# Kernel tuning notes

Hardware: AMD Instinct MI355X
Metric: run time of the kernel (lower is better)

Reference implementation:

```python
import jax, jax.numpy as jnp
import numpy as np

B, P, L = 256, 16, 4
NUM_ENTITY, NUM_NODE = 500000, 512
E, C1, C2 = 128, 512, 256


def setup_inputs() -> dict:
    key = jax.random.key(0)
    ks = jax.random.split(key, 13)
    inp = {
        "start_ids": jax.random.randint(ks[0], (B, P), 0, NUM_ENTITY, dtype=jnp.int32),
        "end_ids": jax.random.randint(ks[1], (B, P), 0, NUM_ENTITY, dtype=jnp.int32),
        "module_ids": jax.random.randint(ks[2], (B, P, L), 0, NUM_NODE, dtype=jnp.int32),
        "counts": jax.random.randint(ks[3], (B, P), 1, 10, dtype=jnp.int32),
        # learned parameters
        "embed": jax.random.normal(ks[4], (NUM_ENTITY, E), dtype=jnp.float32) * 0.02,
        "W": jax.random.normal(ks[5], (NUM_NODE, E, E), dtype=jnp.float32) * (1.0 / np.sqrt(E)),
        "b": jax.random.normal(ks[6], (NUM_NODE, E), dtype=jnp.float32) * 0.01,
        "W1": jax.random.normal(ks[7], (C1, 2 * E), dtype=jnp.float32) * (1.0 / np.sqrt(2 * E)),
        "b1": jnp.zeros((C1,), jnp.float32),
        "W2": jax.random.normal(ks[8], (C2, C1), dtype=jnp.float32) * (1.0 / np.sqrt(C1)),
        "b2": jnp.zeros((C2,), jnp.float32),
        "W3": jax.random.normal(ks[9], (1, C2), dtype=jnp.float32) * (1.0 / np.sqrt(C2)),
        "b3": jnp.zeros((1,), jnp.float32),
    }
    return inp


def reference(start_ids, end_ids, module_ids, counts, embed, W, b, W1, b1, W2, b2, W3, b3):
    # Embed path endpoints: [B, P, E]
    x = embed[start_ids]
    y = embed[end_ids]

    # Apply the same per-node Linear chain to both endpoint embeddings.
    # Scan over the L path steps; gather the step's weight matrices per path.
    def step(carry, mids):  # mids: [B, P]
        x, y = carry
        Wg = W[mids]            # [B, P, E, E] (out, in)
        bg = b[mids]            # [B, P, E]
        x = jnp.einsum('bpi,bpoi->bpo', x, Wg) + bg
        y = jnp.einsum('bpi,bpoi->bpo', y, Wg) + bg
        return (x, y), None

    (x, y), _ = jax.lax.scan(step, (x, y), jnp.transpose(module_ids, (2, 0, 1)))

    feat = jnp.concatenate([x, y], axis=-1)          # [B, P, 2E]
    c = counts.astype(feat.dtype)                    # path multiplicities
    pooled = jnp.einsum('bp,bpf->bf', c, feat) / jnp.sum(c, axis=1, keepdims=True)

    h = jax.nn.relu(pooled @ W1.T + b1)
    h = jax.nn.relu(h @ W2.T + b2)
    out = jax.nn.sigmoid(h @ W3.T + b3)              # [B, 1]
    return out
```

## Files before the change

kernel.cpp:

```cpp
#include <hip/hip_runtime.h>
#include <math.h>

#define BB 256
#define PP 16
#define LL 4
#define EE 128
#define NPATH (BB*PP)
#define NMOD 512
#define CC1 512
#define CC2 256

#define WS_STATE   0
#define WS_CNT     (NPATH*2*EE*4)
#define WS_OFF     (WS_CNT  + LL*NMOD*4)
#define WS_CUR     (WS_OFF  + LL*NMOD*4)
#define WS_LISTS   (WS_CUR  + LL*NMOD*4)
#define WS_POOLED  (WS_LISTS + LL*NPATH*4)
#define WS_H1      (WS_POOLED + BB*2*EE*4)
#define WS_H2      (WS_H1 + BB*CC1*4)
#define WS_END     (WS_H2 + BB*CC2*4)

#define FMA4(A, S, Wv) do{ (A).x=fmaf((S),(Wv).x,(A).x); (A).y=fmaf((S),(Wv).y,(A).y); \
                           (A).z=fmaf((S),(Wv).z,(A).z); (A).w=fmaf((S),(Wv).w,(A).w);}while(0)

__global__ __launch_bounds__(256) void k_zero(int* __restrict__ cnt) {
    cnt[blockIdx.x*256 + threadIdx.x] = 0;
}

__global__ __launch_bounds__(256) void k_seed(
    const int* __restrict__ start_ids, const int* __restrict__ end_ids,
    const int* __restrict__ module_ids, const float* __restrict__ embed,
    float* __restrict__ state, int* __restrict__ cnt)
{
    const int bp = blockIdx.x, t = threadIdx.x;
    const int id = (t < EE) ? start_ids[bp] : end_ids[bp];
    state[(size_t)bp*256 + t] = embed[(size_t)id*EE + (t & (EE-1))];
    if (t < LL) atomicAdd(&cnt[t*NMOD + module_ids[bp*LL + t]], 1);
}

__global__ void k_scan(const int* __restrict__ cnt, int* __restrict__ off,
                       int* __restrict__ cur)
{
    const int l = blockIdx.x, t = threadIdx.x;
    __shared__ int s[NMOD];
    const int c = cnt[l*NMOD + t];
    s[t] = c; __syncthreads();
    for (int d = 1; d < NMOD; d <<= 1) {
        const int v = (t >= d) ? s[t-d] : 0;
        __syncthreads();
        s[t] += v;
        __syncthreads();
    }
    const int excl = s[t] - c;
    off[l*NMOD + t] = excl;
    cur[l*NMOD + t] = excl;
}

__global__ __launch_bounds__(256) void k_scatter(
    const int* __restrict__ module_ids, int* __restrict__ cur,
    int* __restrict__ lists)
{
    const int gid = blockIdx.x*256 + threadIdx.x;
    const int bp = gid >> 2, l = gid & 3;
    const int m = module_ids[gid];
    const int pos = atomicAdd(&cur[l*NMOD + m], 1);
    lists[l*NPATH + pos] = bp;
}

__global__ __launch_bounds__(256) void k_step(
    const int l, const float* __restrict__ W, const float* __restrict__ bvec,
    const int* __restrict__ cnt, const int* __restrict__ off,
    const int* __restrict__ lists, float* __restrict__ state)
{
    __shared__ float Wt[128*64];
    __shared__ float vb[32*128];
    const int m = blockIdx.x, t = threadIdx.x;
    const int n = cnt[l*NMOD + m];
    if (n == 0) return;
    const int* lst = lists + l*NPATH + off[l*NMOD + m];
    const int nr = 2*n;
    const int c = t & 15;
    const int g = t >> 4;
    const float4* state4c = (const float4*)state;

    for (int base = 0; base < nr; base += 32) {
        __syncthreads();
        #pragma unroll
        for (int it = 0; it < 4; ++it) {
            const int flat = it*256 + t;
            const int row = flat >> 5, c4 = flat & 31;
            const int pc = c4 ^ ((row >> 1) & 3);
            float4 v = make_float4(0.f, 0.f, 0.f, 0.f);
            const int r = base + row;
            if (r < nr) {
                const int pv = lst[r >> 1]*2 + (r & 1);
                v = state4c[pv*32 + c4];
            }
            ((float4*)vb)[row*32 + pc] = v;
        }
        for (int ch = 0; ch < 2; ++ch) {
            __syncthreads();
            {
                const int oc = t & 63, kh = t >> 6;
                const float4* Wr = (const float4*)(W + ((size_t)m*128 + ch*64 + oc)*128);
                #pragma unroll
                for (int it = 0; it < 8; ++it) {
                    const int k0 = kh*32 + it*4;
                    const float4 wv = Wr[k0 >> 2];
                    Wt[(k0+0)*64 + oc] = wv.x;
                    Wt[(k0+1)*64 + oc] = wv.y;
                    Wt[(k0+2)*64 + oc] = wv.z;
                    Wt[(k0+3)*64 + oc] = wv.w;
                }
            }
            __syncthreads();
            float4 acc0 = make_float4(0,0,0,0), acc1 = make_float4(0,0,0,0);
            const int row0 = g*2, row1 = g*2 + 1;
            const int sw = g & 3;
            #pragma unroll 4
            for (int k0 = 0; k0 < 128; k0 += 4) {
                const int q = k0 >> 2;
                const float4 w0 = ((const float4*)Wt)[(k0+0)*16 + c];
                const float4 w1 = ((const float4*)Wt)[(k0+1)*16 + c];
                const float4 w2 = ((const float4*)Wt)[(k0+2)*16 + c];
                const float4 w3 = ((const float4*)Wt)[(k0+3)*16 + c];
                const float4 va = ((const float4*)vb)[row0*32 + (q ^ sw)];
                const float4 vy = ((const float4*)vb)[row1*32 + (q ^ sw)];
                FMA4(acc0, va.x, w0); FMA4(acc0, va.y, w1);
                FMA4(acc0, va.z, w2); FMA4(acc0, va.w, w3);
                FMA4(acc1, vy.x, w0); FMA4(acc1, vy.y, w1);
                FMA4(acc1, vy.z, w2); FMA4(acc1, vy.w, w3);
            }
            const float4 bias4 = ((const float4*)(bvec + (size_t)m*128 + ch*64))[c];
            int r = base + row0;
            if (r < nr) {
                const int pv = lst[r >> 1]*2 + (r & 1);
                float4 o = make_float4(acc0.x + bias4.x, acc0.y + bias4.y,
                                       acc0.z + bias4.z, acc0.w + bias4.w);
                ((float4*)state)[pv*32 + ch*16 + c] = o;
            }
            r = base + row1;
            if (r < nr) {
                const int pv = lst[r >> 1]*2 + (r & 1);
                float4 o = make_float4(acc1.x + bias4.x, acc1.y + bias4.y,
                                       acc1.z + bias4.z, acc1.w + bias4.w);
                ((float4*)state)[pv*32 + ch*16 + c] = o;
            }
        }
    }
}

__global__ __launch_bounds__(256) void k_pool(
    const int* __restrict__ counts, const float* __restrict__ state,
    float* __restrict__ pooled)
{
    const int b = blockIdx.x, t = threadIdx.x;
    float acc = 0.f, cs = 0.f;
    #pragma unroll
    for (int p = 0; p < PP; ++p) {
        const float cc = (float)counts[b*PP + p];
        cs += cc;
        acc = fmaf(cc, state[((size_t)(b*PP + p))*256 + t], acc);
    }
    pooled[b*256 + t] = acc / cs;
}

__global__ __launch_bounds__(256) void k_h1(
    const float* __restrict__ pooled, const float* __restrict__ W1,
    const float* __restrict__ b1, float* __restrict__ h1)
{
    __shared__ float ps[8*256];
    const int t = threadIdx.x;
    const int bg = blockIdx.x >> 2, cg = blockIdx.x & 3;
    #pragma unroll
    for (int it = 0; it < 8; ++it) {
        const int flat = it*256 + t;
        ps[flat] = pooled[bg*8*256 + flat];
    }
    __syncthreads();
    const int col = cg*128 + (t & 127);
    const int h = t >> 7;
    const float4* w4 = (const float4*)(W1 + (size_t)col*256);
    const float4* ps4 = (const float4*)ps;
    float a0, a1, a2, a3; a0 = a1 = a2 = a3 = b1[col];
    for (int q = 0; q < 64; ++q) {
        const float4 wv = w4[q];
        const float4 v0 = ps4[(h*4+0)*64 + q];
        const float4 v1 = ps4[(h*4+1)*64 + q];
        const float4 v2 = ps4[(h*4+2)*64 + q];
        const float4 v3 = ps4[(h*4+3)*64 + q];
        a0 = fmaf(wv.x,v0.x, fmaf(wv.y,v0.y, fmaf(wv.z,v0.z, fmaf(wv.w,v0.w, a0))));
        a1 = fmaf(wv.x,v1.x, fmaf(wv.y,v1.y, fmaf(wv.z,v1.z, fmaf(wv.w,v1.w, a1))));
        a2 = fmaf(wv.x,v2.x, fmaf(wv.y,v2.y, fmaf(wv.z,v2.z, fmaf(wv.w,v2.w, a2))));
        a3 = fmaf(wv.x,v3.x, fmaf(wv.y,v3.y, fmaf(wv.z,v3.z, fmaf(wv.w,v3.w, a3))));
    }
    const int b0 = bg*8 + h*4;
    h1[(size_t)(b0+0)*CC1 + col] = fmaxf(a0, 0.f);
    h1[(size_t)(b0+1)*CC1 + col] = fmaxf(a1, 0.f);
    h1[(size_t)(b0+2)*CC1 + col] = fmaxf(a2, 0.f);
    h1[(size_t)(b0+3)*CC1 + col] = fmaxf(a3, 0.f);
}

__global__ __launch_bounds__(256) void k_h2(
    const float* __restrict__ h1, const float* __restrict__ W2,
    const float* __restrict__ b2, float* __restrict__ h2)
{
    __shared__ float hs[8*512];
    const int t = threadIdx.x;
    const int bg = blockIdx.x >> 1, cg = blockIdx.x & 1;
    #pragma unroll
    for (int it = 0; it < 16; ++it) {
        const int flat = it*256 + t;
        hs[flat] = h1[(size_t)bg*8*512 + flat];
    }
    __syncthreads();
    const int col = cg*128 + (t & 127);
    const int h = t >> 7;
    const float4* w4 = (const float4*)(W2 + (size_t)col*512);
    const float4* hs4 = (const float4*)hs;
    float a0, a1, a2, a3; a0 = a1 = a2 = a3 = b2[col];
    for (int q = 0; q < 128; ++q) {
        const float4 wv = w4[q];
        const float4 v0 = hs4[(h*4+0)*128 + q];
        const float4 v1 = hs4[(h*4+1)*128 + q];
        const float4 v2 = hs4[(h*4+2)*128 + q];
        const float4 v3 = hs4[(h*4+3)*128 + q];
        a0 = fmaf(wv.x,v0.x, fmaf(wv.y,v0.y, fmaf(wv.z,v0.z, fmaf(wv.w,v0.w, a0))));
        a1 = fmaf(wv.x,v1.x, fmaf(wv.y,v1.y, fmaf(wv.z,v1.z, fmaf(wv.w,v1.w, a1))));
        a2 = fmaf(wv.x,v2.x, fmaf(wv.y,v2.y, fmaf(wv.z,v2.z, fmaf(wv.w,v2.w, a2))));
        a3 = fmaf(wv.x,v3.x, fmaf(wv.y,v3.y, fmaf(wv.z,v3.z, fmaf(wv.w,v3.w, a3))));
    }
    const int b0 = bg*8 + h*4;
    h2[(size_t)(b0+0)*CC2 + col] = fmaxf(a0, 0.f);
    h2[(size_t)(b0+1)*CC2 + col] = fmaxf(a1, 0.f);
    h2[(size_t)(b0+2)*CC2 + col] = fmaxf(a2, 0.f);
    h2[(size_t)(b0+3)*CC2 + col] = fmaxf(a3, 0.f);
}

__global__ __launch_bounds__(256) void k_out(
    const float* __restrict__ h2, const float* __restrict__ W3,
    const float* __restrict__ b3, float* __restrict__ out)
{
    const int t = threadIdx.x;
    const int b = blockIdx.x*64 + (t >> 2);
    const int q = t & 3;
    const float4* h4 = (const float4*)(h2 + (size_t)b*256);
    const float4* w4 = (const float4*)W3;
    float acc = 0.f;
    #pragma unroll
    for (int i = 0; i < 16; ++i) {
        const int f = q + i*4;
        const float4 hh = h4[f], ww = w4[f];
        acc = fmaf(hh.x,ww.x, fmaf(hh.y,ww.y, fmaf(hh.z,ww.z, fmaf(hh.w,ww.w, acc))));
    }
    acc += __shfl_xor(acc, 1, 4);
    acc += __shfl_xor(acc, 2, 4);
    if (q == 0) out[b] = 1.f / (1.f + expf(-(acc + b3[0])));
}

__global__ __launch_bounds__(256) void fb_path_kernel(
    const int* __restrict__ start_ids, const int* __restrict__ end_ids,
    const int* __restrict__ module_ids,
    const float* __restrict__ embed, const float* __restrict__ W,
    const float* __restrict__ bvec, float* __restrict__ feat_ws)
{
    const int bp = blockIdx.x, t = threadIdx.x;
    __shared__ float bufx[2][EE];
    __shared__ float bufy[2][EE];
    const int sid = start_ids[bp], eid = end_ids[bp];
    if (t < EE) bufx[0][t]      = embed[(size_t)sid*EE + t];
    else        bufy[0][t - EE] = embed[(size_t)eid*EE + (t - EE)];
    __syncthreads();
    const int o = t & (EE - 1);
    int cur = 0;
    for (int l = 0; l < LL; ++l) {
        const int mid = module_ids[bp*LL + l];
        const float*  vin  = (t < EE) ? bufx[cur] : bufy[cur];
        const float4* v4   = (const float4*)vin;
        const float4* wrow = (const float4*)(W + ((size_t)mid*EE + o)*EE);
        float acc = bvec[(size_t)mid*EE + o];
        #pragma unroll 8
        for (int k = 0; k < EE/4; ++k) {
            const float4 wv = wrow[k]; const float4 v = v4[k];
            acc = fmaf(wv.x,v.x, fmaf(wv.y,v.y, fmaf(wv.z,v.z, fmaf(wv.w,v.w, acc))));
        }
        if (t < EE) bufx[1-cur][o] = acc; else bufy[1-cur][o] = acc;
        __syncthreads();
        cur = 1 - cur;
    }
    feat_ws[(size_t)bp*(2*EE) + t] = (t < EE) ? bufx[cur][t] : bufy[cur][t - EE];
}

__global__ __launch_bounds__(256) void fb_mlp_kernel(
    const int* __restrict__ counts, const float* __restrict__ feat_ws,
    const float* __restrict__ W1, const float* __restrict__ b1,
    const float* __restrict__ W2, const float* __restrict__ b2,
    const float* __restrict__ W3, const float* __restrict__ b3,
    float* __restrict__ out)
{
    const int t = threadIdx.x, b0 = blockIdx.x*8;
    __shared__ float pooled[8][2*EE];
    __shared__ float h1s[8][CC1];
    __shared__ float h2s[8][CC2];
    for (int j = 0; j < 8; ++j) {
        const int b = b0 + j;
        float acc = 0.f, csum = 0.f;
        #pragma unroll
        for (int p = 0; p < PP; ++p) {
            const float cc = (float)counts[b*PP + p];
            csum += cc;
            acc = fmaf(cc, feat_ws[(size_t)(b*PP + p)*(2*EE) + t], acc);
        }
        pooled[j][t] = acc / csum;
    }
    __syncthreads();
    for (int rh = 0; rh < 2; ++rh) {
        const int r = t + rh*256;
        float acc[8]; const float bb = b1[r];
        #pragma unroll
        for (int j = 0; j < 8; ++j) acc[j] = bb;
        const float4* w4 = (const float4*)(W1 + (size_t)r*(2*EE));
        for (int k = 0; k < (2*EE)/4; ++k) {
            const float4 wv = w4[k];
            #pragma unroll
            for (int j = 0; j < 8; ++j) {
                const float4 v = ((const float4*)pooled[j])[k];
                acc[j] = fmaf(wv.x,v.x, fmaf(wv.y,v.y, fmaf(wv.z,v.z, fmaf(wv.w,v.w, acc[j]))));
            }
        }
        #pragma unroll
        for (int j = 0; j < 8; ++j) h1s[j][r] = fmaxf(acc[j], 0.f);
    }
    __syncthreads();
    {
        const int r = t;
        float acc[8]; const float bb = b2[r];
        #pragma unroll
        for (int j = 0; j < 8; ++j) acc[j] = bb;
        const float4* w4 = (const float4*)(W2 + (size_t)r*CC1);
        for (int k = 0; k < CC1/4; ++k) {
            const float4 wv = w4[k];
            #pragma unroll
            for (int j = 0; j < 8; ++j) {
                const float4 v = ((const float4*)h1s[j])[k];
                acc[j] = fmaf(wv.x,v.x, fmaf(wv.y,v.y, fmaf(wv.z,v.z, fmaf(wv.w,v.w, acc[j]))));
            }
        }
        #pragma unroll
        for (int j = 0; j < 8; ++j) h2s[j][r] = fmaxf(acc[j], 0.f);
    }
    __syncthreads();
    const int j = t >> 5, k = t & 31;
    float partial = 0.f;
    #pragma unroll
    for (int m = 0; m < CC2; m += 32)
        partial = fmaf(W3[k + m], h2s[j][k + m], partial);
    #pragma unroll
    for (int s = 16; s >= 1; s >>= 1) partial += __shfl_down(partial, s, 32);
    if (k == 0) out[b0 + j] = 1.f / (1.f + expf(-(partial + b3[0])));
}

extern "C" void kernel_launch(void* const* d_in, const int* in_sizes, int n_in,
                              void* d_out, int out_size, void* d_ws, size_t ws_size,
                              hipStream_t stream)
{
    const int*   start_ids  = (const int*)d_in[0];
    const int*   end_ids    = (const int*)d_in[1];
    const int*   module_ids = (const int*)d_in[2];
    const int*   counts     = (const int*)d_in[3];
    const float* embed      = (const float*)d_in[4];
    const float* W          = (const float*)d_in[5];
    const float* bvec       = (const float*)d_in[6];
    const float* W1         = (const float*)d_in[7];
    const float* b1         = (const float*)d_in[8];
    const float* W2         = (const float*)d_in[9];
    const float* b2         = (const float*)d_in[10];
    const float* W3         = (const float*)d_in[11];
    const float* b3         = (const float*)d_in[12];
    float* out = (float*)d_out;
    char*  ws  = (char*)d_ws;

    if (ws_size >= (size_t)WS_END) {
        float* state  = (float*)(ws + WS_STATE);
        int*   cnt    = (int*)(ws + WS_CNT);
        int*   offs   = (int*)(ws + WS_OFF);
        int*   curp   = (int*)(ws + WS_CUR);
        int*   lists  = (int*)(ws + WS_LISTS);
        float* pooled = (float*)(ws + WS_POOLED);
        float* h1     = (float*)(ws + WS_H1);
        float* h2     = (float*)(ws + WS_H2);

        k_zero<<<8, 256, 0, stream>>>(cnt);
        k_seed<<<NPATH, 256, 0, stream>>>(start_ids, end_ids, module_ids, embed, state, cnt);
        k_scan<<<LL, NMOD, 0, stream>>>(cnt, offs, curp);
        k_scatter<<<NPATH*LL/256, 256, 0, stream>>>(module_ids, curp, lists);
        for (int l = 0; l < LL; ++l)
            k_step<<<NMOD, 256, 0, stream>>>(l, W, bvec, cnt, offs, lists, state);
        k_pool<<<BB, 256, 0, stream>>>(counts, state, pooled);
        k_h1<<<128, 256, 0, stream>>>(pooled, W1, b1, h1);
        k_h2<<<64, 256, 0, stream>>>(h1, W2, b2, h2);
        k_out<<<4, 256, 0, stream>>>(h2, W3, b3, out);
    } else {
        float* feat_ws = (float*)d_ws;
        fb_path_kernel<<<NPATH, 256, 0, stream>>>(start_ids, end_ids, module_ids,
                                                  embed, W, bvec, feat_ws);
        fb_mlp_kernel<<<BB/8, 256, 0, stream>>>(counts, feat_ws, W1, b1, W2, b2,
                                                W3, b3, out);
    }
}
```

Measured before the change: 451.8 us.

## Fuse bucketing and MLP kernels, stage bf16 weights once per step block

Replaces the zero/seed-count/scan/scatter kernels with a single per-level bucketing kernel that counts, scans and scatters in shared memory. It also merges pool, h1, h2 and the output layer into one MLP kernel with two batch rows per block. In the step kernel the full 128x128 node weight matrix is converted to bf16 and staged in LDS once, instead of reloading fp32 halves for every 32-row tile, and each thread now computes 4 rows. This cuts launch count and repeated weight traffic, but rounding weights to bf16 reduces accuracy, and the MLP kernel rereads W1/W2 from global memory in each of its 128 blocks.

Result: no change. 446.9 us (-1.1%).

```diff
diff --git a/kernel.cpp b/kernel.cpp
--- a/kernel.cpp
+++ b/kernel.cpp
@@ -13,58 +13,65 @@
 #define WS_STATE   0
 #define WS_CNT     (NPATH*2*EE*4)
 #define WS_OFF     (WS_CNT  + LL*NMOD*4)
-#define WS_CUR     (WS_OFF  + LL*NMOD*4)
-#define WS_LISTS   (WS_CUR  + LL*NMOD*4)
-#define WS_POOLED  (WS_LISTS + LL*NPATH*4)
-#define WS_H1      (WS_POOLED + BB*2*EE*4)
-#define WS_H2      (WS_H1 + BB*CC1*4)
-#define WS_END     (WS_H2 + BB*CC2*4)
+#define WS_LISTS   (WS_OFF  + LL*NMOD*4)
+#define WS_END     (WS_LISTS + LL*NPATH*4)
 
 #define FMA4(A, S, Wv) do{ (A).x=fmaf((S),(Wv).x,(A).x); (A).y=fmaf((S),(Wv).y,(A).y); \
                            (A).z=fmaf((S),(Wv).z,(A).z); (A).w=fmaf((S),(Wv).w,(A).w);}while(0)
 
-__global__ __launch_bounds__(256) void k_zero(int* __restrict__ cnt) {
-    cnt[blockIdx.x*256 + threadIdx.x] = 0;
+__device__ __forceinline__ unsigned short f2bf(float f) {
+    unsigned u = __float_as_uint(f);
+    u = (u + 0x7fffu + ((u >> 16) & 1u)) >> 16;
+    return (unsigned short)u;
+}
+__device__ __forceinline__ float bf2f(unsigned short s) {
+    return __uint_as_float(((unsigned)s) << 16);
+}
+
+__global__ __launch_bounds__(512) void k_bucket(
+    const int* __restrict__ module_ids, int* __restrict__ cnt_g,
+    int* __restrict__ off_g, int* __restrict__ lists)
+{
+    const int l = blockIdx.x, t = threadIdx.x;
+    __shared__ int s[NMOD];
+    __shared__ int pos[NMOD];
+    s[t] = 0;
+    __syncthreads();
+    int mloc[8];
+    #pragma unroll
+    for (int j = 0; j < 8; ++j) {
+        const int bp = j*512 + t;
+        const int m = module_ids[bp*LL + l];
+        mloc[j] = m;
+        atomicAdd(&s[m], 1);
+    }
+    __syncthreads();
+    const int c = s[t];
+    for (int d = 1; d < NMOD; d <<= 1) {
+        const int v = (t >= d) ? s[t-d] : 0;
+        __syncthreads();
+        s[t] += v;
+        __syncthreads();
+    }
+    const int excl = s[t] - c;
+    cnt_g[l*NMOD + t] = c;
+    off_g[l*NMOD + t] = excl;
+    pos[t] = excl;
+    __syncthreads();
+    #pragma unroll
+    for (int j = 0; j < 8; ++j) {
+        const int p = atomicAdd(&pos[mloc[j]], 1);
+        lists[l*NPATH + p] = j*512 + t;
+    }
 }
 
 __global__ __launch_bounds__(256) void k_seed(
     const int* __restrict__ start_ids, const int* __restrict__ end_ids,
-    const int* __restrict__ module_ids, const float* __restrict__ embed,
-    float* __restrict__ state, int* __restrict__ cnt)
+    const float* __restrict__ embed, float* __restrict__ state)
 {
     const int bp = blockIdx.x, t = threadIdx.x;
     const int id = (t < EE) ? start_ids[bp] : end_ids[bp];
     state[(size_t)bp*256 + t] = embed[(size_t)id*EE + (t & (EE-1))];
-    if (t < LL) atomicAdd(&cnt[t*NMOD + module_ids[bp*LL + t]], 1);
-}
-
-__global__ void k_scan(const int* __restrict__ cnt, int* __restrict__ off,
-                       int* __restrict__ cur)
-{
-    const int l = blockIdx.x, t = threadIdx.x;
-    __shared__ int s[NMOD];
-    const int c = cnt[l*NMOD + t];
-    s[t] = c; __syncthreads();
-    for (int d = 1; d < NMOD; d <<= 1) {
-        const int v = (t >= d) ? s[t-d] : 0;
-        __syncthreads();
-        s[t] += v;
-        __syncthreads();
-    }
-    const int excl = s[t] - c;
-    off[l*NMOD + t] = excl;
-    cur[l*NMOD + t] = excl;
-}
-
-__global__ __launch_bounds__(256) void k_scatter(
-    const int* __restrict__ module_ids, int* __restrict__ cur,
-    int* __restrict__ lists)
-{
-    const int gid = blockIdx.x*256 + threadIdx.x;
-    const int bp = gid >> 2, l = gid & 3;
-    const int m = module_ids[gid];
-    const int pos = atomicAdd(&cur[l*NMOD + m], 1);
-    lists[l*NPATH + pos] = bp;
 }
 
 __global__ __launch_bounds__(256) void k_step(
@@ -72,16 +79,31 @@
     const int* __restrict__ cnt, const int* __restrict__ off,
     const int* __restrict__ lists, float* __restrict__ state)
 {
-    __shared__ float Wt[128*64];
+    __shared__ unsigned short Ws[128*128];
     __shared__ float vb[32*128];
     const int m = blockIdx.x, t = threadIdx.x;
     const int n = cnt[l*NMOD + m];
     if (n == 0) return;
+
+    {
+        const int oc = t & 127, kh = t >> 7;
+        const float4* Wr = (const float4*)(W + ((size_t)m*128 + oc)*128 + kh*64);
+        #pragma unroll
+        for (int it = 0; it < 16; ++it) {
+            const float4 wv = Wr[it];
+            const int k0 = kh*64 + it*4;
+            Ws[(k0+0)*128 + oc] = f2bf(wv.x);
+            Ws[(k0+1)*128 + oc] = f2bf(wv.y);
+            Ws[(k0+2)*128 + oc] = f2bf(wv.z);
+            Ws[(k0+3)*128 + oc] = f2bf(wv.w);
+        }
+    }
+
     const int* lst = lists + l*NPATH + off[l*NMOD + m];
     const int nr = 2*n;
-    const int c = t & 15;
-    const int g = t >> 4;
-    const float4* state4c = (const float4*)state;
+    const int cg = t & 31;
+    const int rg = t >> 5;
+    const float4 bias4 = ((const float4*)(bvec + (size_t)m*128))[cg];
 
     for (int base = 0; base < nr; base += 32) {
         __syncthreads();
@@ -89,173 +111,124 @@
         for (int it = 0; it < 4; ++it) {
             const int flat = it*256 + t;
             const int row = flat >> 5, c4 = flat & 31;
-            const int pc = c4 ^ ((row >> 1) & 3);
             float4 v = make_float4(0.f, 0.f, 0.f, 0.f);
             const int r = base + row;
             if (r < nr) {
                 const int pv = lst[r >> 1]*2 + (r & 1);
-                v = state4c[pv*32 + c4];
+                v = ((const float4*)state)[pv*32 + c4];
             }
-            ((float4*)vb)[row*32 + pc] = v;
-        }
-        for (int ch = 0; ch < 2; ++ch) {
-            __syncthreads();
-            {
-                const int oc = t & 63, kh = t >> 6;
-                const float4* Wr = (const float4*)(W + ((size_t)m*128 + ch*64 + oc)*128);
-                #pragma unroll
-                for (int it = 0; it < 8; ++it) {
-                    const int k0 = kh*32 + it*4;
-                    const float4 wv = Wr[k0 >> 2];
-                    Wt[(k0+0)*64 + oc] = wv.x;
-                    Wt[(k0+1)*64 + oc] = wv.y;
-                    Wt[(k0+2)*64 + oc] = wv.z;
-                    Wt[(k0+3)*64 + oc] = wv.w;
-                }
-            }
-            __syncthreads();
-            float4 acc0 = make_float4(0,0,0,0), acc1 = make_float4(0,0,0,0);
-            const int row0 = g*2, row1 = g*2 + 1;
-            const int sw = g & 3;
-            #pragma unroll 4
-            for (int k0 = 0; k0 < 128; k0 += 4) {
-                const int q = k0 >> 2;
-                const float4 w0 = ((const float4*)Wt)[(k0+0)*16 + c];
-                const float4 w1 = ((const float4*)Wt)[(k0+1)*16 + c];
-                const float4 w2 = ((const float4*)Wt)[(k0+2)*16 + c];
-                const float4 w3 = ((const float4*)Wt)[(k0+3)*16 + c];
-                const float4 va = ((const float4*)vb)[row0*32 + (q ^ sw)];
-                const float4 vy = ((const float4*)vb)[row1*32 + (q ^ sw)];
-                FMA4(acc0, va.x, w0); FMA4(acc0, va.y, w1);
-                FMA4(acc0, va.z, w2); FMA4(acc0, va.w, w3);
-                FMA4(acc1, vy.x, w0); FMA4(acc1, vy.y, w1);
-                FMA4(acc1, vy.z, w2); FMA4(acc1, vy.w, w3);
-            }
-            const float4 bias4 = ((const float4*)(bvec + (size_t)m*128 + ch*64))[c];
-            int r = base + row0;
+            ((float4*)vb)[row*32 + c4] = v;
+        }
+        __syncthreads();
+
+        float4 acc0 = make_float4(0,0,0,0), acc1 = make_float4(0,0,0,0);
+        float4 acc2 = make_float4(0,0,0,0), acc3 = make_float4(0,0,0,0);
+        const int r0 = rg*4;
+        #pragma unroll 4
+        for (int k0 = 0; k0 < 128; k0 += 4) {
+            const ushort4 u0 = *(const ushort4*)&Ws[(k0+0)*128 + 4*cg];
+            const ushort4 u1 = *(const ushort4*)&Ws[(k0+1)*128 + 4*cg];
+            const ushort4 u2 = *(const ushort4*)&Ws[(k0+2)*128 + 4*cg];
+            const ushort4 u3 = *(const ushort4*)&Ws[(k0+3)*128 + 4*cg];
+            const int q = k0 >> 2;
+            const float4 va0 = ((const float4*)vb)[(r0+0)*32 + q];
+            const float4 va1 = ((const float4*)vb)[(r0+1)*32 + q];
+            const float4 va2 = ((const float4*)vb)[(r0+2)*32 + q];
+            const float4 va3 = ((const float4*)vb)[(r0+3)*32 + q];
+            const float4 w0 = make_float4(bf2f(u0.x), bf2f(u0.y), bf2f(u0.z), bf2f(u0.w));
+            const float4 w1 = make_float4(bf2f(u1.x), bf2f(u1.y), bf2f(u1.z), bf2f(u1.w));
+            const float4 w2 = make_float4(bf2f(u2.x), bf2f(u2.y), bf2f(u2.z), bf2f(u2.w));
+            const float4 w3 = make_float4(bf2f(u3.x), bf2f(u3.y), bf2f(u3.z), bf2f(u3.w));
+            FMA4(acc0, va0.x, w0); FMA4(acc0, va0.y, w1); FMA4(acc0, va0.z, w2); FMA4(acc0, va0.w, w3);
+            FMA4(acc1, va1.x, w0); FMA4(acc1, va1.y, w1); FMA4(acc1, va1.z, w2); FMA4(acc1, va1.w, w3);
+            FMA4(acc2, va2.x, w0); FMA4(acc2, va2.y, w1); FMA4(acc2, va2.z, w2); FMA4(acc2, va2.w, w3);
+            FMA4(acc3, va3.x, w0); FMA4(acc3, va3.y, w1); FMA4(acc3, va3.z, w2); FMA4(acc3, va3.w, w3);
+        }
+        float4 accs[4] = {acc0, acc1, acc2, acc3};
+        #pragma unroll
+        for (int i = 0; i < 4; ++i) {
+            const int r = base + r0 + i;
             if (r < nr) {
                 const int pv = lst[r >> 1]*2 + (r & 1);
-                float4 o = make_float4(acc0.x + bias4.x, acc0.y + bias4.y,
-                                       acc0.z + bias4.z, acc0.w + bias4.w);
-                ((float4*)state)[pv*32 + ch*16 + c] = o;
+                float4 o = make_float4(accs[i].x + bias4.x, accs[i].y + bias4.y,
+                                       accs[i].z + bias4.z, accs[i].w + bias4.w);
+                ((float4*)state)[pv*32 + cg] = o;
             }
-            r = base + row1;
-            if (r < nr) {
-                const int pv = lst[r >> 1]*2 + (r & 1);
-                float4 o = make_float4(acc1.x + bias4.x, acc1.y + bias4.y,
-                                       acc1.z + bias4.z, acc1.w + bias4.w);
-                ((float4*)state)[pv*32 + ch*16 + c] = o;
-            }
-        }
-    }
-}
-
-__global__ __launch_bounds__(256) void k_pool(
+        }
+    }
+}
+
+__global__ __launch_bounds__(256) void k_mlp(
     const int* __restrict__ counts, const float* __restrict__ state,
-    float* __restrict__ pooled)
-{
-    const int b = blockIdx.x, t = threadIdx.x;
-    float acc = 0.f, cs = 0.f;
-    #pragma unroll
-    for (int p = 0; p < PP; ++p) {
-        const float cc = (float)counts[b*PP + p];
-        cs += cc;
-        acc = fmaf(cc, state[((size_t)(b*PP + p))*256 + t], acc);
-    }
-    pooled[b*256 + t] = acc / cs;
-}
-
-__global__ __launch_bounds__(256) void k_h1(
-    const float* __restrict__ pooled, const float* __restrict__ W1,
-    const float* __restrict__ b1, float* __restrict__ h1)
-{
-    __shared__ float ps[8*256];
+    const float* __restrict__ W1, const float* __restrict__ b1,
+    const float* __restrict__ W2, const float* __restrict__ b2,
+    const float* __restrict__ W3, const float* __restrict__ b3,
+    float* __restrict__ out)
+{
     const int t = threadIdx.x;
-    const int bg = blockIdx.x >> 2, cg = blockIdx.x & 3;
-    #pragma unroll
-    for (int it = 0; it < 8; ++it) {
-        const int flat = it*256 + t;
-        ps[flat] = pooled[bg*8*256 + flat];
-    }
-    __syncthreads();
-    const int col = cg*128 + (t & 127);
-    const int h = t >> 7;
-    const float4* w4 = (const float4*)(W1 + (size_t)col*256);
-    const float4* ps4 = (const float4*)ps;
-    float a0, a1, a2, a3; a0 = a1 = a2 = a3 = b1[col];
-    for (int q = 0; q < 64; ++q) {
-        const float4 wv = w4[q];
-        const float4 v0 = ps4[(h*4+0)*64 + q];
-        const float4 v1 = ps4[(h*4+1)*64 + q];
-        const float4 v2 = ps4[(h*4+2)*64 + q];
-        const float4 v3 = ps4[(h*4+3)*64 + q];
-        a0 = fmaf(wv.x,v0.x, fmaf(wv.y,v0.y, fmaf(wv.z,v0.z, fmaf(wv.w,v0.w, a0))));
-        a1 = fmaf(wv.x,v1.x, fmaf(wv.y,v1.y, fmaf(wv.z,v1.z, fmaf(wv.w,v1.w, a1))));
-        a2 = fmaf(wv.x,v2.x, fmaf(wv.y,v2.y, fmaf(wv.z,v2.z, fmaf(wv.w,v2.w, a2))));
-        a3 = fmaf(wv.x,v3.x, fmaf(wv.y,v3.y, fmaf(wv.z,v3.z, fmaf(wv.w,v3.w, a3))));
-    }
-    const int b0 = bg*8 + h*4;
-    h1[(size_t)(b0+0)*CC1 + col] = fmaxf(a0, 0.f);
-    h1[(size_t)(b0+1)*CC1 + col] = fmaxf(a1, 0.f);
-    h1[(size_t)(b0+2)*CC1 + col] = fmaxf(a2, 0.f);
-    h1[(size_t)(b0+3)*CC1 + col] = fmaxf(a3, 0.f);
-}
-
-__global__ __launch_bounds__(256) void k_h2(
-    const float* __restrict__ h1, const float* __restrict__ W2,
-    const float* __restrict__ b2, float* __restrict__ h2)
-{
-    __shared__ float hs[8*512];
-    const int t = threadIdx.x;
-    const int bg = blockIdx.x >> 1, cg = blockIdx.x & 1;
-    #pragma unroll
-    for (int it = 0; it < 16; ++it) {
-        const int flat = it*256 + t;
-        hs[flat] = h1[(size_t)bg*8*512 + flat];
-    }
-    __syncthreads();
-    const int col = cg*128 + (t & 127);
-    const int h = t >> 7;
-    const float4* w4 = (const float4*)(W2 + (size_t)col*512);
-    const float4* hs4 = (const float4*)hs;
-    float a0, a1, a2, a3; a0 = a1 = a2 = a3 = b2[col];
-    for (int q = 0; q < 128; ++q) {
-        const float4 wv = w4[q];
-        const float4 v0 = hs4[(h*4+0)*128 + q];
-        const float4 v1 = hs4[(h*4+1)*128 + q];
-        const float4 v2 = hs4[(h*4+2)*128 + q];
-        const float4 v3 = hs4[(h*4+3)*128 + q];
-        a0 = fmaf(wv.x,v0.x, fmaf(wv.y,v0.y, fmaf(wv.z,v0.z, fmaf(wv.w,v0.w, a0))));
-        a1 = fmaf(wv.x,v1.x, fmaf(wv.y,v1.y, fmaf(wv.z,v1.z, fmaf(wv.w,v1.w, a1))));
-        a2 = fmaf(wv.x,v2.x, fmaf(wv.y,v2.y, fmaf(wv.z,v2.z, fmaf(wv.w,v2.w, a2))));
-        a3 = fmaf(wv.x,v3.x, fmaf(wv.y,v3.y, fmaf(wv.z,v3.z, fmaf(wv.w,v3.w, a3))));
-    }
-    const int b0 = bg*8 + h*4;
-    h2[(size_t)(b0+0)*CC2 + col] = fmaxf(a0, 0.f);
-    h2[(size_t)(b0+1)*CC2 + col] = fmaxf(a1, 0.f);
-    h2[(size_t)(b0+2)*CC2 + col] = fmaxf(a2, 0.f);
-    h2[(size_t)(b0+3)*CC2 + col] = fmaxf(a3, 0.f);
-}
-
-__global__ __launch_bounds__(256) void k_out(
-    const float* __restrict__ h2, const float* __restrict__ W3,
-    const float* __restrict__ b3, float* __restrict__ out)
-{
-    const int t = threadIdx.x;
-    const int b = blockIdx.x*64 + (t >> 2);
-    const int q = t & 3;
-    const float4* h4 = (const float4*)(h2 + (size_t)b*256);
-    const float4* w4 = (const float4*)W3;
-    float acc = 0.f;
-    #pragma unroll
-    for (int i = 0; i < 16; ++i) {
-        const int f = q + i*4;
-        const float4 hh = h4[f], ww = w4[f];
-        acc = fmaf(hh.x,ww.x, fmaf(hh.y,ww.y, fmaf(hh.z,ww.z, fmaf(hh.w,ww.w, acc))));
-    }
-    acc += __shfl_xor(acc, 1, 4);
-    acc += __shfl_xor(acc, 2, 4);
-    if (q == 0) out[b] = 1.f / (1.f + expf(-(acc + b3[0])));
+    const int b0 = blockIdx.x * 2;
+    __shared__ float pl[2][256];
+    __shared__ float h1s[2][CC1];
+    __shared__ float h2s[2][CC2];
+    __shared__ float red[256];
+
+    #pragma unroll
+    for (int r = 0; r < 2; ++r) {
+        const int b = b0 + r;
+        float acc = 0.f, cs = 0.f;
+        #pragma unroll
+        for (int p = 0; p < PP; ++p) {
+            const float cc = (float)counts[b*PP + p];
+            cs += cc;
+            acc = fmaf(cc, state[((size_t)(b*PP + p))*256 + t], acc);
+        }
+        pl[r][t] = acc / cs;
+    }
+    __syncthreads();
+
+    #pragma unroll
+    for (int hh = 0; hh < 2; ++hh) {
+        const int col = t + hh*256;
+        const float4* w4 = (const float4*)(W1 + (size_t)col*256);
+        float a0 = b1[col], a1 = a0;
+        for (int q = 0; q < 64; ++q) {
+            const float4 wv = w4[q];
+            const float4 v0 = ((const float4*)pl[0])[q];
+            const float4 v1 = ((const float4*)pl[1])[q];
+            a0 = fmaf(wv.x,v0.x, fmaf(wv.y,v0.y, fmaf(wv.z,v0.z, fmaf(wv.w,v0.w, a0))));
+            a1 = fmaf(wv.x,v1.x, fmaf(wv.y,v1.y, fmaf(wv.z,v1.z, fmaf(wv.w,v1.w, a1))));
+        }
+        h1s[0][col] = fmaxf(a0, 0.f);
+        h1s[1][col] = fmaxf(a1, 0.f);
+    }
+    __syncthreads();
+
+    {
+        const float4* w4 = (const float4*)(W2 + (size_t)t*512);
+        float a0 = b2[t], a1 = a0;
+        for (int q = 0; q < 128; ++q) {
+            const float4 wv = w4[q];
+            const float4 v0 = ((const float4*)h1s[0])[q];
+            const float4 v1 = ((const float4*)h1s[1])[q];
+            a0 = fmaf(wv.x,v0.x, fmaf(wv.y,v0.y, fmaf(wv.z,v0.z, fmaf(wv.w,v0.w, a0))));
+            a1 = fmaf(wv.x,v1.x, fmaf(wv.y,v1.y, fmaf(wv.z,v1.z, fmaf(wv.w,v1.w, a1))));
+        }
+        h2s[0][t] = fmaxf(a0, 0.f);
+        h2s[1][t] = fmaxf(a1, 0.f);
+    }
+    __syncthreads();
+
+    {
+        const int r = t >> 7, k = t & 127;
+        red[t] = fmaf(W3[k], h2s[r][k], W3[k+128] * h2s[r][k+128]);
+        for (int s = 64; s > 0; s >>= 1) {
+            __syncthreads();
+            if ((t & 127) < s) red[t] += red[t + s];
+        }
+        __syncthreads();
+        if ((t & 127) == 0)
+            out[b0 + r] = 1.f / (1.f + expf(-(red[t] + b3[0])));
+    }
 }
 
 __global__ __launch_bounds__(256) void fb_path_kernel(
@@ -381,25 +354,16 @@
     char*  ws  = (char*)d_ws;
 
     if (ws_size >= (size_t)WS_END) {
-        float* state  = (float*)(ws + WS_STATE);
-        int*   cnt    = (int*)(ws + WS_CNT);
-        int*   offs   = (int*)(ws + WS_OFF);
-        int*   curp   = (int*)(ws + WS_CUR);
-        int*   lists  = (int*)(ws + WS_LISTS);
-        float* pooled = (float*)(ws + WS_POOLED);
-        float* h1     = (float*)(ws + WS_H1);
-        float* h2     = (float*)(ws + WS_H2);
-
-        k_zero<<<8, 256, 0, stream>>>(cnt);
-        k_seed<<<NPATH, 256, 0, stream>>>(start_ids, end_ids, module_ids, embed, state, cnt);
-        k_scan<<<LL, NMOD, 0, stream>>>(cnt, offs, curp);
-        k_scatter<<<NPATH*LL/256, 256, 0, stream>>>(module_ids, curp, lists);
+        float* state = (float*)(ws + WS_STATE);
+        int*   cnt   = (int*)(ws + WS_CNT);
+        int*   offs  = (int*)(ws + WS_OFF);
+        int*   lists = (int*)(ws + WS_LISTS);
+
+        k_bucket<<<LL, 512, 0, stream>>>(module_ids, cnt, offs, lists);
+        k_seed<<<NPATH, 256, 0, stream>>>(start_ids, end_ids, embed, state);
         for (int l = 0; l < LL; ++l)
             k_step<<<NMOD, 256, 0, stream>>>(l, W, bvec, cnt, offs, lists, state);
-        k_pool<<<BB, 256, 0, stream>>>(counts, state, pooled);
-        k_h1<<<128, 256, 0, stream>>>(pooled, W1, b1, h1);
-        k_h2<<<64, 256, 0, stream>>>(h1, W2, b2, h2);
-        k_out<<<4, 256, 0, stream>>>(h2, W3, b3, out);
+        k_mlp<<<BB/2, 256, 0, stream>>>(counts, state, W1, b1, W2, b2, W3, b3, out);
     } else {
         float* feat_ws = (float*)d_ws;
         fb_path_kernel<<<NPATH, 256, 0, stream>>>(start_ids, end_ids, module_ids,
```
